# Optimization experiments

Hardware: AMD Instinct MI355X
Metric: run time of the kernel (lower is better)

The kernel has to match this reference:

```python
import jax, jax.numpy as jnp
import numpy as np

B, S, D_MODEL = 8, 2048, 512
G, V = 2, 320          # num_groups, num_vars
CV_DIM = 256 // G      # proj_dim // num_groups = 128
TAU = 2.0


def setup_inputs() -> dict:
    key = jax.random.key(0)
    k1, k2, k3, k4, k5 = jax.random.split(key, 5)
    hidden_states = jax.random.normal(k1, (B, S, D_MODEL), dtype=jnp.float32)
    # Linear(d_model -> G*V); store as (in, out) for direct matmul
    W = jax.random.normal(k2, (D_MODEL, G * V), dtype=jnp.float32) * (1.0 / np.sqrt(D_MODEL))
    b = jax.random.normal(k3, (G * V,), dtype=jnp.float32) * 0.01
    codevectors = jax.random.normal(k4, (1, G * V, CV_DIM), dtype=jnp.float32)
    # pre-sampled Gumbel(0,1) noise, shape (B*S*G, V)
    u = jax.random.uniform(k5, (B * S * G, V), dtype=jnp.float32,
                           minval=1e-10, maxval=1.0)
    gumbels = -jnp.log(-jnp.log(u))
    return {"hidden_states": hidden_states, "W": W, "b": b,
            "codevectors": codevectors, "gumbels": gumbels}


def reference(hidden_states, W, b, codevectors, gumbels):
    Bs, Ss, _ = hidden_states.shape
    N = Bs * Ss
    # weight projection: (B,S,D) @ (D,G*V) -> (B,S,G*V)
    logits = hidden_states @ W + b
    logits = logits.reshape(N * G, V).astype(jnp.float32)

    # gumbel-softmax, hard=True with straight-through
    y_soft = jax.nn.softmax((logits + gumbels) / TAU, axis=-1)  # (N*G, V)
    idx = jnp.argmax(y_soft, axis=-1)
    y_hard = jax.nn.one_hot(idx, V, dtype=y_soft.dtype)
    codevector_probs = y_hard - jax.lax.stop_gradient(y_soft) + y_soft

    # perplexity from the (noise-free) soft distribution
    soft_dist = jax.nn.softmax(logits.reshape(N, G, V), axis=-1)
    marginal = soft_dist.mean(axis=0)                            # (G, V)
    perplexity = jnp.exp(-jnp.sum(marginal * jnp.log(marginal + 1e-7),
                                  axis=-1)).sum()

    # codebook lookup as weighted sum (equivalent to one-hot gather)
    cv = codevectors.reshape(G, V, CV_DIM)
    probs = codevector_probs.reshape(N, G, V)
    out = jnp.einsum('ngv,gvd->ngd', probs, cv)                  # (N, G, d)
    out = out.reshape(Bs, Ss, G * CV_DIM)
    return out, perplexity
```

## Files before the change

### kernel.cpp

```cpp
#include <hip/hip_runtime.h>

#define M_ROWS 16384
#define K_DIM  512
#define N_COLS 640
#define V_CODES 320
#define CV_DIM 128

typedef _Float16 half8 __attribute__((ext_vector_type(8)));
typedef _Float16 half4v __attribute__((ext_vector_type(4)));
typedef float floatx4 __attribute__((ext_vector_type(4)));

__device__ inline void gll16(const void* g, void* l) {
    __builtin_amdgcn_global_load_lds(
        (const __attribute__((address_space(1))) void*)g,
        (__attribute__((address_space(3))) void*)l, 16, 0, 0);
}

__global__ __launch_bounds__(256)
void prepW(const float* __restrict__ W, _Float16* __restrict__ Wt,
           float* __restrict__ marginal) {
    __shared__ float tile[32][33];
    const int b = blockIdx.x, t = threadIdx.x;
    if (b == 320) {
        for (int i = t; i < 640; i += 256) marginal[i] = 0.f;
        return;
    }
    const int n0 = (b % 20) * 32, k0 = (b / 20) * 32;
    {
        const int kk = t >> 3, nn4 = (t & 7) << 2;
        const float4 w = *(const float4*)(W + (size_t)(k0 + kk) * 640 + n0 + nn4);
        tile[kk][nn4 + 0] = w.x; tile[kk][nn4 + 1] = w.y;
        tile[kk][nn4 + 2] = w.z; tile[kk][nn4 + 3] = w.w;
    }
    __syncthreads();
    {
        const int nn = t >> 3, kk4 = (t & 7) << 2;
        half4v h = {(_Float16)tile[kk4 + 0][nn], (_Float16)tile[kk4 + 1][nn],
                    (_Float16)tile[kk4 + 2][nn], (_Float16)tile[kk4 + 3][nn]};
        *(half4v*)(Wt + (size_t)(n0 + nn) * 512 + k0 + kk4) = h;
    }
}

__global__ __launch_bounds__(256, 2)
void fused(const float* __restrict__ A, const _Float16* __restrict__ Bt,
           const float* __restrict__ bias, const float* __restrict__ gum,
           const float* __restrict__ cv, float* __restrict__ out,
           float* __restrict__ marginal) {
    __shared__ _Float16 As[2][64 * 32];
    __shared__ _Float16 Bs[2][320 * 32];
    __shared__ float smarg[320];
    const int t = threadIdx.x;
    const int wave = t >> 6, lane = t & 63;
    const int bm = blockIdx.x, g = blockIdx.y;
    const int mi = wave;
    const int c = lane & 15, kq = lane >> 4;

    for (int i = t; i < 320; i += 256) smarg[i] = 0.f;

    floatx4 acc[20];
#pragma unroll
    for (int nt = 0; nt < 20; ++nt) acc[nt] = (floatx4){0.f, 0.f, 0.f, 0.f};

    const int am = t >> 2, ad = t & 3;
    const int a_wr = am * 64 + ((ad ^ (am & 3)) << 4);
    const float* Aptr = A + (size_t)(bm * 64 + am) * 512 + ad * 8;

    const _Float16* Bg = Bt + (size_t)g * V_CODES * K_DIM;

    auto STAGE = [&](int buf, int k0) {
        const float4 av0 = *(const float4*)(Aptr + k0);
        const float4 av1 = *(const float4*)(Aptr + k0 + 4);
#pragma unroll
        for (int s = 0; s < 5; ++s) {
            const int q = t + 256 * s;
            const int n = q >> 2, j = q & 3;
            gll16(Bg + (size_t)n * 512 + k0 + ((j ^ (n & 3)) << 3),
                  (char*)(&Bs[buf][0]) + q * 16);
        }
        const half8 h = {(_Float16)av0.x, (_Float16)av0.y, (_Float16)av0.z,
                         (_Float16)av0.w, (_Float16)av1.x, (_Float16)av1.y,
                         (_Float16)av1.z, (_Float16)av1.w};
        *(half8*)((char*)(&As[buf][0]) + a_wr) = h;
    };

    STAGE(0, 0);
    __syncthreads();

    for (int kt = 0; kt < 16; ++kt) {
        const int cur = kt & 1;
        if (kt < 15) STAGE(cur ^ 1, (kt + 1) * 32);
        const int ra = mi * 16 + c;
        const half8 af = *(const half8*)((const char*)(&As[cur][0]) +
                          ra * 64 + ((kq ^ (ra & 3)) << 4));
#pragma unroll
        for (int nt = 0; nt < 20; ++nt) {
            const int rb = nt * 16 + c;
            const half8 bf = *(const half8*)((const char*)(&Bs[cur][0]) +
                              rb * 64 + ((kq ^ (rb & 3)) << 4));
            acc[nt] = __builtin_amdgcn_mfma_f32_16x16x32_f16(af, bf, acc[nt], 0, 0, 0);
        }
        __syncthreads();
    }

    float bcol[20];
#pragma unroll
    for (int nt = 0; nt < 20; ++nt) bcol[nt] = bias[g * V_CODES + nt * 16 + c];

    float mcontrib[20];
#pragma unroll
    for (int nt = 0; nt < 20; ++nt) mcontrib[nt] = 0.f;

#pragma unroll
    for (int rg = 0; rg < 4; ++rg) {
        const int ntok = bm * 64 + mi * 16 + kq * 4 + rg;
        float lg[20];
#pragma unroll
        for (int nt = 0; nt < 20; ++nt) lg[nt] = acc[nt][rg] + bcol[nt];
        const float* gr = gum + ((size_t)ntok * 2 + g) * V_CODES + c;
        float gv[20];
#pragma unroll
        for (int nt = 0; nt < 20; ++nt) gv[nt] = gr[nt * 16];
        float best = -1e30f; int bidx = 0;
#pragma unroll
        for (int nt = 0; nt < 20; ++nt) {
            const float nz = lg[nt] + gv[nt];
            const int v = nt * 16 + c;
            if (nz > best) { best = nz; bidx = v; }
        }
#pragma unroll
        for (int mask = 1; mask <= 8; mask <<= 1) {
            const float ob = __shfl_xor(best, mask);
            const int   oi = __shfl_xor(bidx, mask);
            if (ob > best || (ob == best && oi < bidx)) { best = ob; bidx = oi; }
        }
        float s = 0.f;
#pragma unroll
        for (int nt = 0; nt < 20; ++nt) { lg[nt] = __expf(lg[nt]); s += lg[nt]; }
#pragma unroll
        for (int mask = 1; mask <= 8; mask <<= 1) s += __shfl_xor(s, mask);
        const float inv = 1.f / s;
#pragma unroll
        for (int nt = 0; nt < 20; ++nt) mcontrib[nt] += lg[nt] * inv;
        const float4* cvp = (const float4*)(cv + ((size_t)g * V_CODES + bidx) * CV_DIM)
                            + c * 2;
        const float4 v0 = cvp[0], v1 = cvp[1];
        float4* op = (float4*)(out + (size_t)ntok * 256 + g * CV_DIM) + c * 2;
        op[0] = v0; op[1] = v1;
    }

#pragma unroll
    for (int nt = 0; nt < 20; ++nt) {
        mcontrib[nt] += __shfl_xor(mcontrib[nt], 16);
        mcontrib[nt] += __shfl_xor(mcontrib[nt], 32);
    }
    if (lane < 16) {
#pragma unroll
        for (int nt = 0; nt < 20; ++nt)
            atomicAdd(&smarg[nt * 16 + c], mcontrib[nt]);
    }
    __syncthreads();
    for (int i = t; i < 320; i += 256)
        atomicAdd(marginal + g * V_CODES + i, smarg[i]);
}

__global__ __launch_bounds__(640)
void finalize(const float* __restrict__ marginal, float* __restrict__ perp_out) {
    __shared__ float terms[640];
    __shared__ float gsum[2];
    const int t = threadIdx.x;

    const float m = marginal[t] * (1.0f / (float)M_ROWS);
    terms[t] = -m * __logf(m + 1e-7f);
    __syncthreads();

    if (t < 128) {
        const int g = t >> 6, lane = t & 63;
        float e = 0.f;
#pragma unroll
        for (int j = 0; j < 5; ++j) e += terms[g * V_CODES + lane + 64 * j];
#pragma unroll
        for (int off = 32; off; off >>= 1) e += __shfl_down(e, off);
        if (lane == 0) gsum[g] = e;
    }
    __syncthreads();
    if (t == 0) perp_out[0] = __expf(gsum[0]) + __expf(gsum[1]);
}

extern "C" void kernel_launch(void* const* d_in, const int* in_sizes, int n_in,
                              void* d_out, int out_size, void* d_ws, size_t ws_size,
                              hipStream_t stream) {
    (void)in_sizes; (void)n_in; (void)out_size; (void)ws_size;
    const float* hs = (const float*)d_in[0];
    const float* W  = (const float*)d_in[1];
    const float* bi = (const float*)d_in[2];
    const float* cv = (const float*)d_in[3];
    const float* gu = (const float*)d_in[4];
    float* out = (float*)d_out;

    _Float16* Wt       = (_Float16*)d_ws;
    float*    marginal = (float*)(Wt + (size_t)N_COLS * K_DIM);

    prepW<<<321, 256, 0, stream>>>(W, Wt, marginal);
    fused<<<dim3(256, 2), 256, 0, stream>>>(hs, Wt, bi, gu, cv, out, marginal);
    finalize<<<1, 640, 0, stream>>>(marginal, out + (size_t)M_ROWS * 256);
}
```

Before: 49.01 us.

## Stage full A tile in LDS and stream B fragments from global into registers

The fused GEMM kernel now converts and stores the block's full 64x512 A tile in LDS once, instead of double-buffering 32-wide K slices. Each wave owns 80 of the 320 output columns and loads its B fragments straight from global memory into registers with one-step prefetch, which removes the per-iteration barriers and the LDS staging of B. Because the columns are split across waves, argmax and softmax sums are now combined across waves through shared memory before the codebook gather. Marginal atomics go straight to global memory. The 64KB A tile in LDS may limit how many blocks fit per CU, and B is re-read from global or L2 by every block.

Measured after the change: 64.56 us. +31.7%, slower.

```diff
diff --git a/kernel.cpp b/kernel.cpp
--- a/kernel.cpp
+++ b/kernel.cpp
@@ -9,12 +9,6 @@
 typedef _Float16 half8 __attribute__((ext_vector_type(8)));
 typedef _Float16 half4v __attribute__((ext_vector_type(4)));
 typedef float floatx4 __attribute__((ext_vector_type(4)));
-
-__device__ inline void gll16(const void* g, void* l) {
-    __builtin_amdgcn_global_load_lds(
-        (const __attribute__((address_space(1))) void*)g,
-        (__attribute__((address_space(3))) void*)l, 16, 0, 0);
-}
 
 __global__ __launch_bounds__(256)
 void prepW(const float* __restrict__ W, _Float16* __restrict__ Wt,
@@ -46,121 +40,172 @@
            const float* __restrict__ bias, const float* __restrict__ gum,
            const float* __restrict__ cv, float* __restrict__ out,
            float* __restrict__ marginal) {
-    __shared__ _Float16 As[2][64 * 32];
-    __shared__ _Float16 Bs[2][320 * 32];
-    __shared__ float smarg[320];
+    __shared__ _Float16 As[64 * 512];
+    __shared__ float wbest[4][64];
+    __shared__ int   wbidx[4][64];
+    __shared__ float wsum[4][64];
+    __shared__ int   fbidx[64];
+    __shared__ float finv[64];
+
     const int t = threadIdx.x;
     const int wave = t >> 6, lane = t & 63;
     const int bm = blockIdx.x, g = blockIdx.y;
-    const int mi = wave;
     const int c = lane & 15, kq = lane >> 4;
 
-    for (int i = t; i < 320; i += 256) smarg[i] = 0.f;
-
-    floatx4 acc[20];
-#pragma unroll
-    for (int nt = 0; nt < 20; ++nt) acc[nt] = (floatx4){0.f, 0.f, 0.f, 0.f};
-
-    const int am = t >> 2, ad = t & 3;
-    const int a_wr = am * 64 + ((ad ^ (am & 3)) << 4);
-    const float* Aptr = A + (size_t)(bm * 64 + am) * 512 + ad * 8;
-
-    const _Float16* Bg = Bt + (size_t)g * V_CODES * K_DIM;
-
-    auto STAGE = [&](int buf, int k0) {
-        const float4 av0 = *(const float4*)(Aptr + k0);
-        const float4 av1 = *(const float4*)(Aptr + k0 + 4);
-#pragma unroll
-        for (int s = 0; s < 5; ++s) {
-            const int q = t + 256 * s;
-            const int n = q >> 2, j = q & 3;
-            gll16(Bg + (size_t)n * 512 + k0 + ((j ^ (n & 3)) << 3),
-                  (char*)(&Bs[buf][0]) + q * 16);
-        }
-        const half8 h = {(_Float16)av0.x, (_Float16)av0.y, (_Float16)av0.z,
-                         (_Float16)av0.w, (_Float16)av1.x, (_Float16)av1.y,
-                         (_Float16)av1.z, (_Float16)av1.w};
-        *(half8*)((char*)(&As[buf][0]) + a_wr) = h;
-    };
-
-    STAGE(0, 0);
-    __syncthreads();
-
+    {
+        const int am = t >> 2;
+        const int kb = (t & 3) * 128;
+        const float* Ap = A + (size_t)(bm * 64 + am) * 512 + kb;
+#pragma unroll
+        for (int i = 0; i < 16; ++i) {
+            const float4 v0 = *(const float4*)(Ap + i * 8);
+            const float4 v1 = *(const float4*)(Ap + i * 8 + 4);
+            const half8 h = {(_Float16)v0.x, (_Float16)v0.y, (_Float16)v0.z,
+                             (_Float16)v0.w, (_Float16)v1.x, (_Float16)v1.y,
+                             (_Float16)v1.z, (_Float16)v1.w};
+            const int chunk = ((kb >> 3) + i) ^ (am & 7);
+            *(half8*)((char*)As + am * 1024 + chunk * 16) = h;
+        }
+    }
+    __syncthreads();
+
+    floatx4 acc[4][5];
+#pragma unroll
+    for (int mt = 0; mt < 4; ++mt)
+#pragma unroll
+        for (int nt = 0; nt < 5; ++nt) acc[mt][nt] = (floatx4){0.f, 0.f, 0.f, 0.f};
+
+    const _Float16* Bg = Bt + (size_t)g * V_CODES * K_DIM
+                            + (size_t)(wave * 80 + c) * K_DIM + kq * 8;
+
+    half8 bcur[5], bnxt[5], af[4];
+#pragma unroll
+    for (int nt = 0; nt < 5; ++nt)
+        bcur[nt] = *(const half8*)(Bg + (size_t)nt * 16 * K_DIM);
+
+#pragma unroll 2
     for (int kt = 0; kt < 16; ++kt) {
-        const int cur = kt & 1;
-        if (kt < 15) STAGE(cur ^ 1, (kt + 1) * 32);
-        const int ra = mi * 16 + c;
-        const half8 af = *(const half8*)((const char*)(&As[cur][0]) +
-                          ra * 64 + ((kq ^ (ra & 3)) << 4));
-#pragma unroll
-        for (int nt = 0; nt < 20; ++nt) {
-            const int rb = nt * 16 + c;
-            const half8 bf = *(const half8*)((const char*)(&Bs[cur][0]) +
-                              rb * 64 + ((kq ^ (rb & 3)) << 4));
-            acc[nt] = __builtin_amdgcn_mfma_f32_16x16x32_f16(af, bf, acc[nt], 0, 0, 0);
-        }
-        __syncthreads();
-    }
-
-    float bcol[20];
-#pragma unroll
-    for (int nt = 0; nt < 20; ++nt) bcol[nt] = bias[g * V_CODES + nt * 16 + c];
-
-    float mcontrib[20];
-#pragma unroll
-    for (int nt = 0; nt < 20; ++nt) mcontrib[nt] = 0.f;
-
-#pragma unroll
-    for (int rg = 0; rg < 4; ++rg) {
-        const int ntok = bm * 64 + mi * 16 + kq * 4 + rg;
-        float lg[20];
-#pragma unroll
-        for (int nt = 0; nt < 20; ++nt) lg[nt] = acc[nt][rg] + bcol[nt];
-        const float* gr = gum + ((size_t)ntok * 2 + g) * V_CODES + c;
-        float gv[20];
-#pragma unroll
-        for (int nt = 0; nt < 20; ++nt) gv[nt] = gr[nt * 16];
-        float best = -1e30f; int bidx = 0;
-#pragma unroll
-        for (int nt = 0; nt < 20; ++nt) {
-            const float nz = lg[nt] + gv[nt];
-            const int v = nt * 16 + c;
-            if (nz > best) { best = nz; bidx = v; }
-        }
-#pragma unroll
-        for (int mask = 1; mask <= 8; mask <<= 1) {
-            const float ob = __shfl_xor(best, mask);
-            const int   oi = __shfl_xor(bidx, mask);
-            if (ob > best || (ob == best && oi < bidx)) { best = ob; bidx = oi; }
-        }
-        float s = 0.f;
-#pragma unroll
-        for (int nt = 0; nt < 20; ++nt) { lg[nt] = __expf(lg[nt]); s += lg[nt]; }
-#pragma unroll
-        for (int mask = 1; mask <= 8; mask <<= 1) s += __shfl_xor(s, mask);
-        const float inv = 1.f / s;
-#pragma unroll
-        for (int nt = 0; nt < 20; ++nt) mcontrib[nt] += lg[nt] * inv;
-        const float4* cvp = (const float4*)(cv + ((size_t)g * V_CODES + bidx) * CV_DIM)
+        if (kt < 15) {
+#pragma unroll
+            for (int nt = 0; nt < 5; ++nt)
+                bnxt[nt] = *(const half8*)(Bg + (size_t)nt * 16 * K_DIM
+                                           + (kt + 1) * 32);
+        }
+#pragma unroll
+        for (int mt = 0; mt < 4; ++mt) {
+            const int ra = mt * 16 + c;
+            const int chunk = (kt * 4 + kq) ^ (ra & 7);
+            af[mt] = *(const half8*)((const char*)As + ra * 1024 + chunk * 16);
+        }
+#pragma unroll
+        for (int mt = 0; mt < 4; ++mt)
+#pragma unroll
+            for (int nt = 0; nt < 5; ++nt)
+                acc[mt][nt] = __builtin_amdgcn_mfma_f32_16x16x32_f16(
+                    af[mt], bcur[nt], acc[mt][nt], 0, 0, 0);
+#pragma unroll
+        for (int nt = 0; nt < 5; ++nt) bcur[nt] = bnxt[nt];
+    }
+
+    float bcol[5];
+#pragma unroll
+    for (int nt = 0; nt < 5; ++nt)
+        bcol[nt] = bias[g * V_CODES + wave * 80 + nt * 16 + c];
+#pragma unroll
+    for (int mt = 0; mt < 4; ++mt)
+#pragma unroll
+        for (int nt = 0; nt < 5; ++nt)
+#pragma unroll
+            for (int rg = 0; rg < 4; ++rg) acc[mt][nt][rg] += bcol[nt];
+
+    __syncthreads();
+
+#pragma unroll
+    for (int mt = 0; mt < 4; ++mt) {
+#pragma unroll
+        for (int rg = 0; rg < 4; ++rg) {
+            const int r = mt * 16 + kq * 4 + rg;
+            const float* gr = gum + ((size_t)(bm * 64 + r) * 2 + g) * V_CODES
+                              + wave * 80 + c;
+            float best = -1e30f; int bidx = 0;
+#pragma unroll
+            for (int nt = 0; nt < 5; ++nt) {
+                const float nz = acc[mt][nt][rg] + gr[nt * 16];
+                const int v = wave * 80 + nt * 16 + c;
+                if (nz > best) { best = nz; bidx = v; }
+            }
+#pragma unroll
+            for (int mask = 1; mask <= 8; mask <<= 1) {
+                const float ob = __shfl_xor(best, mask);
+                const int   oi = __shfl_xor(bidx, mask);
+                if (ob > best || (ob == best && oi < bidx)) { best = ob; bidx = oi; }
+            }
+            float s = 0.f;
+#pragma unroll
+            for (int nt = 0; nt < 5; ++nt) {
+                const float e = __expf(acc[mt][nt][rg]);
+                acc[mt][nt][rg] = e;
+                s += e;
+            }
+#pragma unroll
+            for (int mask = 1; mask <= 8; mask <<= 1) s += __shfl_xor(s, mask);
+            if (c == 0) {
+                wbest[wave][r] = best;
+                wbidx[wave][r] = bidx;
+                wsum[wave][r]  = s;
+            }
+        }
+    }
+    __syncthreads();
+
+    if (t < 64) {
+        float best = wbest[0][t]; int bi = wbidx[0][t];
+        float s = wsum[0][t];
+#pragma unroll
+        for (int w = 1; w < 4; ++w) {
+            const float ob = wbest[w][t]; const int oi = wbidx[w][t];
+            if (ob > best || (ob == best && oi < bi)) { best = ob; bi = oi; }
+            s += wsum[w][t];
+        }
+        fbidx[t] = bi;
+        finv[t] = 1.f / s;
+    }
+    __syncthreads();
+
+    float mcon[5];
+#pragma unroll
+    for (int nt = 0; nt < 5; ++nt) mcon[nt] = 0.f;
+#pragma unroll
+    for (int mt = 0; mt < 4; ++mt) {
+#pragma unroll
+        for (int rg = 0; rg < 4; ++rg) {
+            const float iv = finv[mt * 16 + kq * 4 + rg];
+#pragma unroll
+            for (int nt = 0; nt < 5; ++nt) mcon[nt] += acc[mt][nt][rg] * iv;
+        }
+    }
+#pragma unroll
+    for (int nt = 0; nt < 5; ++nt) {
+        mcon[nt] += __shfl_xor(mcon[nt], 16);
+        mcon[nt] += __shfl_xor(mcon[nt], 32);
+    }
+    if (lane < 16) {
+#pragma unroll
+        for (int nt = 0; nt < 5; ++nt)
+            atomicAdd(marginal + g * V_CODES + wave * 80 + nt * 16 + c, mcon[nt]);
+    }
+
+#pragma unroll
+    for (int rr = 0; rr < 4; ++rr) {
+        const int row = wave * 16 + kq * 4 + rr;
+        const int bi = fbidx[row];
+        const float4* cvp = (const float4*)(cv + ((size_t)g * V_CODES + bi) * CV_DIM)
                             + c * 2;
         const float4 v0 = cvp[0], v1 = cvp[1];
-        float4* op = (float4*)(out + (size_t)ntok * 256 + g * CV_DIM) + c * 2;
+        float4* op = (float4*)(out + (size_t)(bm * 64 + row) * 256 + g * CV_DIM)
+                     + c * 2;
         op[0] = v0; op[1] = v1;
     }
-
-#pragma unroll
-    for (int nt = 0; nt < 20; ++nt) {
-        mcontrib[nt] += __shfl_xor(mcontrib[nt], 16);
-        mcontrib[nt] += __shfl_xor(mcontrib[nt], 32);
-    }
-    if (lane < 16) {
-#pragma unroll
-        for (int nt = 0; nt < 20; ++nt)
-            atomicAdd(&smarg[nt * 16 + c], mcontrib[nt]);
-    }
-    __syncthreads();
-    for (int i = t; i < 320; i += 256)
-        atomicAdd(marginal + g * V_CODES + i, smarg[i]);
 }
 
 __global__ __launch_bounds__(640)
```

## Halve row tile, split vocab across waves, replicate marginal accumulators

Applied to the files above, without the earlier changes.

The fused kernel now handles 32 rows per block instead of 64, and splits the 320 codes between wave pairs. Argmax and softmax sums are combined across waves through shared memory. This doubles the grid to 1024 blocks and cuts accumulator registers to allow 3 blocks per SM, which should raise occupancy. Global atomics on the marginal are spread over 8 replicas that finalize sums, which reduces contention. In exchange, each block reloads the full B tile for fewer rows, so W traffic rises, and the extra block-level syncs add overhead.

Result: slower. 57.45 us (+17.2%).

```diff
diff --git a/kernel.cpp b/kernel.cpp
--- a/kernel.cpp
+++ b/kernel.cpp
@@ -5,6 +5,7 @@
 #define N_COLS 640
 #define V_CODES 320
 #define CV_DIM 128
+#define NREP 8
 
 typedef _Float16 half8 __attribute__((ext_vector_type(8)));
 typedef _Float16 half4v __attribute__((ext_vector_type(4)));
@@ -18,11 +19,11 @@
 
 __global__ __launch_bounds__(256)
 void prepW(const float* __restrict__ W, _Float16* __restrict__ Wt,
-           float* __restrict__ marginal) {
+           float* __restrict__ marg8) {
     __shared__ float tile[32][33];
     const int b = blockIdx.x, t = threadIdx.x;
     if (b == 320) {
-        for (int i = t; i < 640; i += 256) marginal[i] = 0.f;
+        for (int i = t; i < NREP * 640; i += 256) marg8[i] = 0.f;
         return;
     }
     const int n0 = (b % 20) * 32, k0 = (b / 20) * 32;
@@ -41,35 +42,40 @@
     }
 }
 
-__global__ __launch_bounds__(256, 2)
+__global__ __launch_bounds__(256, 3)
 void fused(const float* __restrict__ A, const _Float16* __restrict__ Bt,
            const float* __restrict__ bias, const float* __restrict__ gum,
            const float* __restrict__ cv, float* __restrict__ out,
-           float* __restrict__ marginal) {
-    __shared__ _Float16 As[2][64 * 32];
+           float* __restrict__ marg8) {
     __shared__ _Float16 Bs[2][320 * 32];
+    __shared__ _Float16 As[2][32 * 32];
     __shared__ float smarg[320];
+    __shared__ float wbest[2][32];
+    __shared__ float wsum[2][32];
+    __shared__ int   wbidx[2][32];
+    __shared__ int   fbidx[32];
+    __shared__ float finv[32];
+
     const int t = threadIdx.x;
     const int wave = t >> 6, lane = t & 63;
     const int bm = blockIdx.x, g = blockIdx.y;
-    const int mi = wave;
+    const int mi = wave >> 1, nh = wave & 1;
     const int c = lane & 15, kq = lane >> 4;
 
     for (int i = t; i < 320; i += 256) smarg[i] = 0.f;
 
-    floatx4 acc[20];
-#pragma unroll
-    for (int nt = 0; nt < 20; ++nt) acc[nt] = (floatx4){0.f, 0.f, 0.f, 0.f};
-
-    const int am = t >> 2, ad = t & 3;
-    const int a_wr = am * 64 + ((ad ^ (am & 3)) << 4);
-    const float* Aptr = A + (size_t)(bm * 64 + am) * 512 + ad * 8;
+    floatx4 acc[10];
+#pragma unroll
+    for (int nt = 0; nt < 10; ++nt) acc[nt] = (floatx4){0.f, 0.f, 0.f, 0.f};
+
+    const int arow = t >> 3, ak4 = t & 7;
+    const int a_wr = arow * 64 + ((((ak4 >> 1) ^ (arow & 3))) << 4) + (ak4 & 1) * 8;
+    const float* Aptr = A + (size_t)(bm * 32 + arow) * 512 + ak4 * 4;
 
     const _Float16* Bg = Bt + (size_t)g * V_CODES * K_DIM;
 
     auto STAGE = [&](int buf, int k0) {
-        const float4 av0 = *(const float4*)(Aptr + k0);
-        const float4 av1 = *(const float4*)(Aptr + k0 + 4);
+        const float4 av = *(const float4*)(Aptr + k0);
 #pragma unroll
         for (int s = 0; s < 5; ++s) {
             const int q = t + 256 * s;
@@ -77,10 +83,9 @@
             gll16(Bg + (size_t)n * 512 + k0 + ((j ^ (n & 3)) << 3),
                   (char*)(&Bs[buf][0]) + q * 16);
         }
-        const half8 h = {(_Float16)av0.x, (_Float16)av0.y, (_Float16)av0.z,
-                         (_Float16)av0.w, (_Float16)av1.x, (_Float16)av1.y,
-                         (_Float16)av1.z, (_Float16)av1.w};
-        *(half8*)((char*)(&As[buf][0]) + a_wr) = h;
+        const half4v h = {(_Float16)av.x, (_Float16)av.y,
+                          (_Float16)av.z, (_Float16)av.w};
+        *(half4v*)((char*)(&As[buf][0]) + a_wr) = h;
     };
 
     STAGE(0, 0);
@@ -93,8 +98,8 @@
         const half8 af = *(const half8*)((const char*)(&As[cur][0]) +
                           ra * 64 + ((kq ^ (ra & 3)) << 4));
 #pragma unroll
-        for (int nt = 0; nt < 20; ++nt) {
-            const int rb = nt * 16 + c;
+        for (int nt = 0; nt < 10; ++nt) {
+            const int rb = nh * 160 + nt * 16 + c;
             const half8 bf = *(const half8*)((const char*)(&Bs[cur][0]) +
                               rb * 64 + ((kq ^ (rb & 3)) << 4));
             acc[nt] = __builtin_amdgcn_mfma_f32_16x16x32_f16(af, bf, acc[nt], 0, 0, 0);
@@ -102,29 +107,25 @@
         __syncthreads();
     }
 
-    float bcol[20];
-#pragma unroll
-    for (int nt = 0; nt < 20; ++nt) bcol[nt] = bias[g * V_CODES + nt * 16 + c];
-
-    float mcontrib[20];
-#pragma unroll
-    for (int nt = 0; nt < 20; ++nt) mcontrib[nt] = 0.f;
+    float bcol[10];
+#pragma unroll
+    for (int nt = 0; nt < 10; ++nt)
+        bcol[nt] = bias[g * V_CODES + nh * 160 + nt * 16 + c];
+#pragma unroll
+    for (int nt = 0; nt < 10; ++nt)
+#pragma unroll
+        for (int rg = 0; rg < 4; ++rg) acc[nt][rg] += bcol[nt];
 
 #pragma unroll
     for (int rg = 0; rg < 4; ++rg) {
-        const int ntok = bm * 64 + mi * 16 + kq * 4 + rg;
-        float lg[20];
-#pragma unroll
-        for (int nt = 0; nt < 20; ++nt) lg[nt] = acc[nt][rg] + bcol[nt];
-        const float* gr = gum + ((size_t)ntok * 2 + g) * V_CODES + c;
-        float gv[20];
-#pragma unroll
-        for (int nt = 0; nt < 20; ++nt) gv[nt] = gr[nt * 16];
+        const int rloc = mi * 16 + kq * 4 + rg;
+        const float* gr = gum + ((size_t)(bm * 32 + rloc) * 2 + g) * V_CODES
+                          + nh * 160 + c;
         float best = -1e30f; int bidx = 0;
 #pragma unroll
-        for (int nt = 0; nt < 20; ++nt) {
-            const float nz = lg[nt] + gv[nt];
-            const int v = nt * 16 + c;
+        for (int nt = 0; nt < 10; ++nt) {
+            const float nz = acc[nt][rg] + gr[nt * 16];
+            const int v = nh * 160 + nt * 16 + c;
             if (nz > best) { best = nz; bidx = v; }
         }
 #pragma unroll
@@ -135,41 +136,77 @@
         }
         float s = 0.f;
 #pragma unroll
-        for (int nt = 0; nt < 20; ++nt) { lg[nt] = __expf(lg[nt]); s += lg[nt]; }
+        for (int nt = 0; nt < 10; ++nt) {
+            const float e = __expf(acc[nt][rg]);
+            acc[nt][rg] = e;
+            s += e;
+        }
 #pragma unroll
         for (int mask = 1; mask <= 8; mask <<= 1) s += __shfl_xor(s, mask);
-        const float inv = 1.f / s;
-#pragma unroll
-        for (int nt = 0; nt < 20; ++nt) mcontrib[nt] += lg[nt] * inv;
-        const float4* cvp = (const float4*)(cv + ((size_t)g * V_CODES + bidx) * CV_DIM)
-                            + c * 2;
-        const float4 v0 = cvp[0], v1 = cvp[1];
-        float4* op = (float4*)(out + (size_t)ntok * 256 + g * CV_DIM) + c * 2;
-        op[0] = v0; op[1] = v1;
-    }
-
-#pragma unroll
-    for (int nt = 0; nt < 20; ++nt) {
-        mcontrib[nt] += __shfl_xor(mcontrib[nt], 16);
-        mcontrib[nt] += __shfl_xor(mcontrib[nt], 32);
+        if (c == 0) {
+            wbest[nh][rloc] = best;
+            wbidx[nh][rloc] = bidx;
+            wsum[nh][rloc]  = s;
+        }
+    }
+    __syncthreads();
+
+    if (t < 32) {
+        float best = wbest[0][t]; int bi = wbidx[0][t];
+        const float ob = wbest[1][t]; const int oi = wbidx[1][t];
+        if (ob > best || (ob == best && oi < bi)) { best = ob; bi = oi; }
+        fbidx[t] = bi;
+        finv[t] = 1.f / (wsum[0][t] + wsum[1][t]);
+    }
+    __syncthreads();
+
+    float mcon[10];
+#pragma unroll
+    for (int nt = 0; nt < 10; ++nt) mcon[nt] = 0.f;
+#pragma unroll
+    for (int rg = 0; rg < 4; ++rg) {
+        const float iv = finv[mi * 16 + kq * 4 + rg];
+#pragma unroll
+        for (int nt = 0; nt < 10; ++nt) mcon[nt] += acc[nt][rg] * iv;
+    }
+#pragma unroll
+    for (int nt = 0; nt < 10; ++nt) {
+        mcon[nt] += __shfl_xor(mcon[nt], 16);
+        mcon[nt] += __shfl_xor(mcon[nt], 32);
     }
     if (lane < 16) {
 #pragma unroll
-        for (int nt = 0; nt < 20; ++nt)
-            atomicAdd(&smarg[nt * 16 + c], mcontrib[nt]);
+        for (int nt = 0; nt < 10; ++nt)
+            atomicAdd(&smarg[nh * 160 + nt * 16 + c], mcon[nt]);
     }
     __syncthreads();
     for (int i = t; i < 320; i += 256)
-        atomicAdd(marginal + g * V_CODES + i, smarg[i]);
+        atomicAdd(marg8 + (size_t)(bm & (NREP - 1)) * 640 + g * V_CODES + i,
+                  smarg[i]);
+
+    {
+        const int rowl = wave * 8 + (lane >> 3);
+        const int p = lane & 7;
+        const int bi = fbidx[rowl];
+        const float4* cvp = (const float4*)(cv + ((size_t)g * V_CODES + bi) * CV_DIM)
+                            + p * 4;
+        const float4 v0 = cvp[0], v1 = cvp[1], v2 = cvp[2], v3 = cvp[3];
+        float4* op = (float4*)(out + (size_t)(bm * 32 + rowl) * 256 + g * CV_DIM)
+                     + p * 4;
+        op[0] = v0; op[1] = v1; op[2] = v2; op[3] = v3;
+    }
 }
 
 __global__ __launch_bounds__(640)
-void finalize(const float* __restrict__ marginal, float* __restrict__ perp_out) {
+void finalize(const float* __restrict__ marg8, float* __restrict__ perp_out) {
     __shared__ float terms[640];
     __shared__ float gsum[2];
     const int t = threadIdx.x;
 
-    const float m = marginal[t] * (1.0f / (float)M_ROWS);
+    float s = 0.f;
+#pragma unroll
+    for (int k = 0; k < NREP; ++k) s += marg8[k * 640 + t];
+    const float m = s * (1.0f / (float)M_ROWS);
     terms[t] = -m * __logf(m + 1e-7f);
     __syncthreads();
 
@@ -197,10 +234,10 @@
     const float* gu = (const float*)d_in[4];
     float* out = (float*)d_out;
 
-    _Float16* Wt       = (_Float16*)d_ws;
-    float*    marginal = (float*)(Wt + (size_t)N_COLS * K_DIM);
-
-    prepW<<<321, 256, 0, stream>>>(W, Wt, marginal);
-    fused<<<dim3(256, 2), 256, 0, stream>>>(hs, Wt, bi, gu, cv, out, marginal);
-    finalize<<<1, 640, 0, stream>>>(marginal, out + (size_t)M_ROWS * 256);
-}
+    _Float16* Wt    = (_Float16*)d_ws;
+    float*    marg8 = (float*)(Wt + (size_t)N_COLS * K_DIM);
+
+    prepW<<<321, 256, 0, stream>>>(W, Wt, marg8);
+    fused<<<dim3(512, 2), 256, 0, stream>>>(hs, Wt, bi, gu, cv, out, marg8);
+    finalize<<<1, 640, 0, stream>>>(marg8, out + (size_t)M_ROWS * 256);
+}
```

## Stage logits in LDS as fp16 to free registers and raise occupancy

Applied to the files above, without the earlier changes.

After the MFMA main loop, biased logits are written into an LDS buffer that reuses the GEMM staging memory, so the accumulator registers can be released before the softmax and argmax epilogue. Gumbel noise for all four rows is loaded up front to batch the global reads, and the launch bound moves from two to three blocks per CU. The aim is to cut register pressure and hide epilogue latency. The logits are stored at fp16 precision, which can change argmax results and perplexity. The grid of 512 blocks may already fit at two blocks per CU, and the tighter register cap may cause spills.

Result: slower. 50.72 us (+3.5%).

```diff
diff --git a/kernel.cpp b/kernel.cpp
--- a/kernel.cpp
+++ b/kernel.cpp
@@ -5,6 +5,7 @@
 #define N_COLS 640
 #define V_CODES 320
 #define CV_DIM 128
+#define LSTRIDE 330
 
 typedef _Float16 half8 __attribute__((ext_vector_type(8)));
 typedef _Float16 half4v __attribute__((ext_vector_type(4)));
@@ -41,13 +42,17 @@
     }
 }
 
-__global__ __launch_bounds__(256, 2)
+union SMemG {
+    struct { _Float16 Bs[2][320 * 32]; _Float16 As[2][64 * 32]; } g;
+    _Float16 L[64 * LSTRIDE];
+};
+
+__global__ __launch_bounds__(256, 3)
 void fused(const float* __restrict__ A, const _Float16* __restrict__ Bt,
            const float* __restrict__ bias, const float* __restrict__ gum,
            const float* __restrict__ cv, float* __restrict__ out,
            float* __restrict__ marginal) {
-    __shared__ _Float16 As[2][64 * 32];
-    __shared__ _Float16 Bs[2][320 * 32];
+    __shared__ SMemG sm;
     __shared__ float smarg[320];
     const int t = threadIdx.x;
     const int wave = t >> 6, lane = t & 63;
@@ -75,12 +80,12 @@
             const int q = t + 256 * s;
             const int n = q >> 2, j = q & 3;
             gll16(Bg + (size_t)n * 512 + k0 + ((j ^ (n & 3)) << 3),
-                  (char*)(&Bs[buf][0]) + q * 16);
+                  (char*)(&sm.g.Bs[buf][0]) + q * 16);
         }
         const half8 h = {(_Float16)av0.x, (_Float16)av0.y, (_Float16)av0.z,
                          (_Float16)av0.w, (_Float16)av1.x, (_Float16)av1.y,
                          (_Float16)av1.z, (_Float16)av1.w};
-        *(half8*)((char*)(&As[buf][0]) + a_wr) = h;
+        *(half8*)((char*)(&sm.g.As[buf][0]) + a_wr) = h;
     };
 
     STAGE(0, 0);
@@ -90,12 +95,12 @@
         const int cur = kt & 1;
         if (kt < 15) STAGE(cur ^ 1, (kt + 1) * 32);
         const int ra = mi * 16 + c;
-        const half8 af = *(const half8*)((const char*)(&As[cur][0]) +
+        const half8 af = *(const half8*)((const char*)(&sm.g.As[cur][0]) +
                           ra * 64 + ((kq ^ (ra & 3)) << 4));
 #pragma unroll
         for (int nt = 0; nt < 20; ++nt) {
             const int rb = nt * 16 + c;
-            const half8 bf = *(const half8*)((const char*)(&Bs[cur][0]) +
+            const half8 bf = *(const half8*)((const char*)(&sm.g.Bs[cur][0]) +
                               rb * 64 + ((kq ^ (rb & 3)) << 4));
             acc[nt] = __builtin_amdgcn_mfma_f32_16x16x32_f16(af, bf, acc[nt], 0, 0, 0);
         }
@@ -105,25 +110,38 @@
     float bcol[20];
 #pragma unroll
     for (int nt = 0; nt < 20; ++nt) bcol[nt] = bias[g * V_CODES + nt * 16 + c];
-
-    float mcontrib[20];
-#pragma unroll
-    for (int nt = 0; nt < 20; ++nt) mcontrib[nt] = 0.f;
-
+#pragma unroll
+    for (int rg = 0; rg < 4; ++rg) {
+        const int row = mi * 16 + kq * 4 + rg;
+#pragma unroll
+        for (int nt = 0; nt < 20; ++nt)
+            sm.L[row * LSTRIDE + nt * 16 + c] = (_Float16)(acc[nt][rg] + bcol[nt]);
+    }
+
+    float gv[4][20];
 #pragma unroll
     for (int rg = 0; rg < 4; ++rg) {
         const int ntok = bm * 64 + mi * 16 + kq * 4 + rg;
+        const float* gr = gum + ((size_t)ntok * 2 + g) * V_CODES + c;
+#pragma unroll
+        for (int nt = 0; nt < 20; ++nt) gv[rg][nt] = gr[nt * 16];
+    }
+
+    float mcontrib[20];
+#pragma unroll
+    for (int nt = 0; nt < 20; ++nt) mcontrib[nt] = 0.f;
+
+#pragma unroll
+    for (int rg = 0; rg < 4; ++rg) {
+        const int row = mi * 16 + kq * 4 + rg;
         float lg[20];
 #pragma unroll
-        for (int nt = 0; nt < 20; ++nt) lg[nt] = acc[nt][rg] + bcol[nt];
-        const float* gr = gum + ((size_t)ntok * 2 + g) * V_CODES + c;
-        float gv[20];
-#pragma unroll
-        for (int nt = 0; nt < 20; ++nt) gv[nt] = gr[nt * 16];
+        for (int nt = 0; nt < 20; ++nt)
+            lg[nt] = (float)sm.L[row * LSTRIDE + nt * 16 + c];
         float best = -1e30f; int bidx = 0;
 #pragma unroll
         for (int nt = 0; nt < 20; ++nt) {
-            const float nz = lg[nt] + gv[nt];
+            const float nz = lg[nt] + gv[rg][nt];
             const int v = nt * 16 + c;
             if (nz > best) { best = nz; bidx = v; }
         }
@@ -141,6 +159,7 @@
         const float inv = 1.f / s;
 #pragma unroll
         for (int nt = 0; nt < 20; ++nt) mcontrib[nt] += lg[nt] * inv;
+        const int ntok = bm * 64 + row;
         const float4* cvp = (const float4*)(cv + ((size_t)g * V_CODES + bidx) * CV_DIM)
                             + c * 2;
         const float4 v0 = cvp[0], v1 = cvp[1];
```
